# Kernel tuning notes

Measured on AMD Instinct MI355X. Metric: run time of the kernel, lower is better.

## Reference

```python
import jax, jax.numpy as jnp
import numpy as np

MAX_DEG = 6
N_ATOMS = 500000
BATCH = 1024
F_IN = 75
# atoms are sorted by degree (DeepChem ConvMol convention); counts for degree 0..6
DEG_COUNTS = [20000, 80000, 150000, 150000, 75000, 20000, 5000]
OFF = np.cumsum([0] + DEG_COUNTS)


def setup_inputs():
    key = jax.random.key(0)
    ks = jax.random.split(key, 20)

    def p(k, shape):
        return jax.random.normal(k, shape, jnp.float32) * 0.05

    inp = {}
    inp["atom_features"] = jax.random.normal(ks[0], (N_ATOMS, F_IN), jnp.float32)
    inp["membership"] = jax.random.randint(ks[1], (N_ATOMS,), 0, BATCH)
    for d in range(1, MAX_DEG + 1):
        inp[f"adj{d}"] = jax.random.randint(ks[1 + d], (DEG_COUNTS[d], d), 0, N_ATOMS)
    inp["gc1_Wn"] = p(ks[8], (MAX_DEG, F_IN, 64))
    inp["gc1_Ws"] = p(ks[9], (MAX_DEG + 1, F_IN, 64))
    inp["gc1_b"] = jnp.zeros((MAX_DEG + 1, 64), jnp.float32)
    inp["gc2_Wn"] = p(ks[10], (MAX_DEG, 64, 64))
    inp["gc2_Ws"] = p(ks[11], (MAX_DEG + 1, 64, 64))
    inp["gc2_b"] = jnp.zeros((MAX_DEG + 1, 64), jnp.float32)
    inp["bn1_gamma"] = jnp.ones((64,), jnp.float32)
    inp["bn1_beta"] = jnp.zeros((64,), jnp.float32)
    inp["bn1_mean"] = jnp.zeros((64,), jnp.float32)
    inp["bn1_var"] = jnp.ones((64,), jnp.float32)
    inp["bn3_gamma"] = jnp.ones((128,), jnp.float32)
    inp["bn3_beta"] = jnp.zeros((128,), jnp.float32)
    inp["bn3_mean"] = jnp.zeros((128,), jnp.float32)
    inp["bn3_var"] = jnp.ones((128,), jnp.float32)
    inp["d1_W"] = p(ks[12], (64, 128))
    inp["d1_b"] = jnp.zeros((128,), jnp.float32)
    inp["d2_W"] = p(ks[13], (256, 64))
    inp["d2_b"] = jnp.zeros((64,), jnp.float32)
    inp["d3_W"] = p(ks[14], (64, 1))
    inp["d3_b"] = jnp.zeros((1,), jnp.float32)
    return inp


def batch_norm(x, gamma, beta, mean, var, eps=1e-3):
    # keras BatchNormalization in inference mode (eps = keras default 1e-3)
    return gamma * (x - mean) * jax.lax.rsqrt(var + eps) + beta


def graph_conv(feat, adjs, Wn, Ws, b):
    # degree-0 atoms: self transform only
    outs = [feat[OFF[0]:OFF[1]] @ Ws[0] + b[0]]
    for d in range(1, MAX_DEG + 1):
        summed = feat[adjs[d - 1]].sum(axis=1)        # [n_d, F] neighbor-sum gather
        self_a = feat[OFF[d]:OFF[d + 1]]              # [n_d, F] atoms of degree d
        outs.append(summed @ Wn[d - 1] + self_a @ Ws[d] + b[d])
    return jnp.tanh(jnp.concatenate(outs, axis=0))


def graph_pool(feat, adjs):
    outs = [feat[OFF[0]:OFF[1]]]                      # degree-0: passthrough
    for d in range(1, MAX_DEG + 1):
        gathered = feat[adjs[d - 1]]                  # [n_d, d, F]
        self_a = feat[OFF[d]:OFF[d + 1]][:, None, :]  # [n_d, 1, F]
        outs.append(jnp.max(jnp.concatenate([self_a, gathered], axis=1), axis=1))
    return jnp.concatenate(outs, axis=0)


def graph_gather(feat, membership):
    s = jax.ops.segment_sum(feat, membership, num_segments=BATCH)
    m = jax.ops.segment_max(feat, membership, num_segments=BATCH)
    return jnp.tanh(jnp.concatenate([s, m], axis=1))  # [BATCH, 2F]


def reference(atom_features, membership, adj1, adj2, adj3, adj4, adj5, adj6,
              gc1_Wn, gc1_Ws, gc1_b, gc2_Wn, gc2_Ws, gc2_b,
              bn1_gamma, bn1_beta, bn1_mean, bn1_var,
              bn3_gamma, bn3_beta, bn3_mean, bn3_var,
              d1_W, d1_b, d2_W, d2_b, d3_W, d3_b):
    adjs = [adj1, adj2, adj3, adj4, adj5, adj6]
    h = graph_conv(atom_features, adjs, gc1_Wn, gc1_Ws, gc1_b)
    h = batch_norm(h, bn1_gamma, bn1_beta, bn1_mean, bn1_var)
    h = graph_pool(h, adjs)
    h = graph_conv(h, adjs, gc2_Wn, gc2_Ws, gc2_b)
    # NOTE: source code reuses self.batch_norm1 after gc2 (batch_norm2 is unused)
    h = batch_norm(h, bn1_gamma, bn1_beta, bn1_mean, bn1_var)
    h = graph_pool(h, adjs)
    h = jnp.tanh(h @ d1_W + d1_b)
    h = batch_norm(h, bn3_gamma, bn3_beta, bn3_mean, bn3_var)
    g = graph_gather(h, membership)                   # [BATCH, 256]
    g = jax.nn.sigmoid(g @ d2_W + d2_b)
    return g @ d3_W + d3_b                            # [BATCH, 1]
```

## Files before the change

### kernel.cpp

```cpp
#include <hip/hip_runtime.h>
#include <hip/hip_fp16.h>
#include <math.h>


struct AdjPtrs { const int* p[6]; };

typedef _Float16 f16x8 __attribute__((ext_vector_type(8)));
typedef float f32x4 __attribute__((ext_vector_type(4)));

__device__ __forceinline__ float tanh_fast(float x) {
  float ax = fabsf(x);
  float r = __expf(-2.f * ax);
  float t = 1.f - 2.f * r * __builtin_amdgcn_rcpf(1.f + r);
  return copysignf(t, x);
}

__device__ __forceinline__ f16x8 max8(f16x8 a, f16x8 b) {
  #pragma unroll
  for (int i = 0; i < 8; i++) a[i] = (a[i] > b[i]) ? a[i] : b[i];
  return a;
}

__global__ __launch_bounds__(256) void k_zero_hist(int* __restrict__ hist) {
  int i = blockIdx.x * 256 + threadIdx.x;
  if (i < 1024) hist[i] = 0;
}

__global__ __launch_bounds__(256) void k_hist(const int* __restrict__ mem, int* __restrict__ hist) {
  __shared__ int lh[1024];
  int tid = threadIdx.x;
  for (int i = tid; i < 1024; i += 256) lh[i] = 0;
  __syncthreads();
  int stride = gridDim.x * 256;
  for (int i = blockIdx.x * 256 + tid; i < 500000; i += stride)
    atomicAdd(&lh[mem[i]], 1);
  __syncthreads();
  for (int i = tid; i < 1024; i += 256) {
    int v = lh[i];
    if (v) atomicAdd(&hist[i], v);
  }
}

__global__ __launch_bounds__(1024) void k_scan(const int* __restrict__ hist,
                                               int* __restrict__ start,
                                               int* __restrict__ cursor) {
  __shared__ int sc[1024];
  int t = threadIdx.x;
  int h = hist[t];
  sc[t] = h;
  __syncthreads();
  for (int off = 1; off < 1024; off <<= 1) {
    int v = (t >= off) ? sc[t - off] : 0;
    __syncthreads();
    sc[t] += v;
    __syncthreads();
  }
  int ex = sc[t] - h;
  start[t] = ex;
  cursor[t] = ex;
}

__global__ __launch_bounds__(256) void k_scatter(const int* __restrict__ mem,
                                                 int* __restrict__ cursor,
                                                 int* __restrict__ list) {
  int i = blockIdx.x * 256 + threadIdx.x;
  if (i < 500000) {
    int pos = atomicAdd(&cursor[mem[i]], 1);
    list[pos] = i;
  }
}

__global__ __launch_bounds__(256) void k_prep(const float* __restrict__ feat,
                                              __half2* __restrict__ featH2) {
  int i = blockIdx.x * 256 + threadIdx.x;
  int a = i / 40;
  int jp = i - a * 40;
  int kk = jp * 2;
  float v0 = (kk < 75) ? feat[(size_t)a * 75 + kk] : 0.f;
  float v1 = (kk + 1 < 75) ? feat[(size_t)a * 75 + kk + 1] : 0.f;
  featH2[i] = __floats2half2_rn(v0, v1);
}

__global__ __launch_bounds__(256) void k_prep_w(
    const float* __restrict__ Ws1, const float* __restrict__ Wn1,
    const float* __restrict__ Ws2, const float* __restrict__ Wn2,
    __half* __restrict__ W1H, __half* __restrict__ W2H) {
  int i = blockIdx.x * 256 + threadIdx.x;
  if (i < 71680) {
    int d = i / 10240, r = i - d * 10240;
    int j = r & 7, lane = (r >> 3) & 63, t = r >> 9;
    int n = (t & 3) * 16 + (lane & 15);
    int k = (t >> 2) * 32 + (lane >> 4) * 8 + j;
    float v = 0.f;
    if (k < 75) v = Ws1[d * 4800 + k * 64 + n];
    else if (k >= 80 && k < 155 && d > 0) v = Wn1[(d - 1) * 4800 + (k - 80) * 64 + n];
    W1H[i] = __float2half(v);
  } else {
    int i2 = i - 71680;
    int d = i2 / 8192, r = i2 - d * 8192;
    int j = r & 7, lane = (r >> 3) & 63, t = r >> 9;
    int n = (t & 3) * 16 + (lane & 15);
    int k = (t >> 2) * 32 + (lane >> 4) * 8 + j;
    float v = 0.f;
    if (k < 64) v = Ws2[d * 4096 + k * 64 + n];
    else if (d > 0) v = Wn2[(d - 1) * 4096 + (k - 64) * 64 + n];
    W2H[i2] = __float2half(v);
  }
}

__global__ __launch_bounds__(256) void k_prep_d1(const float* __restrict__ W,
                                                 __half* __restrict__ D1H) {
  int i = blockIdx.x * 256 + threadIdx.x;
  int n = i >> 6, k = i & 63;
  float v = W[k * 128 + n];
  __half hi = __float2half(v);
  D1H[i] = hi;
  D1H[8192 + i] = __float2half(v - __half2float(hi));
}

template<int FP, int NCH, int D>
__device__ __forceinline__ void gcm_run(
    const __half* __restrict__ featH, const int* __restrict__ adj_g,
    int abase, int na, const f16x8* __restrict__ Wf,
    const float* __restrict__ bias_d,
    const float* __restrict__ bng, const float* __restrict__ bnb,
    const float* __restrict__ bnm, const float* __restrict__ bnv,
    __half* __restrict__ out) {
  int tid = threadIdx.x;
  int lane = tid & 63, w = tid >> 6;
  int ln = lane & 15, q = lane >> 4;

  int ar[2][D > 0 ? D : 1];
  if (D > 0) {
    #pragma unroll
    for (int ms = 0; ms < 2; ms++) {
      int m = w * 32 + ms * 16 + ln;
      bool ok = (m < na);
      #pragma unroll
      for (int e = 0; e < D; e++)
        ar[ms][e] = ok ? adj_g[m * D + e] : 0;
    }
  }

  f32x4 acc[2][4];
  #pragma unroll
  for (int ns = 0; ns < 4; ns++) {
    float bj = bias_d[ns * 16 + ln];
    acc[0][ns] = (f32x4){bj, bj, bj, bj};
    acc[1][ns] = acc[0][ns];
  }

  #pragma unroll
  for (int c = 0; c < NCH; c++) {
    int ksg = c * 32 + q * 8;
    f16x8 af[2];
    #pragma unroll
    for (int ms = 0; ms < 2; ms++) {
      int m = w * 32 + ms * 16 + ln;
      if (ksg < FP) {
        af[ms] = *(const f16x8*)(featH + (size_t)(abase + m) * FP + ksg);
      } else if (D > 0) {
        int kb = ksg - FP;
        f16x8 v = *(const f16x8*)(featH + (size_t)ar[ms][0] * FP + kb);
        #pragma unroll
        for (int e = 1; e < D; e++) {
          f16x8 u = *(const f16x8*)(featH + (size_t)ar[ms][e] * FP + kb);
          v = v + u;
        }
        af[ms] = v;
      } else {
        af[ms] = (f16x8){};
      }
    }
    #pragma unroll
    for (int ns = 0; ns < 4; ns++) {
      f16x8 bf = Wf[(c * 4 + ns) * 64 + lane];
      acc[0][ns] = __builtin_amdgcn_mfma_f32_16x16x32_f16(af[0], bf, acc[0][ns], 0, 0, 0);
      acc[1][ns] = __builtin_amdgcn_mfma_f32_16x16x32_f16(af[1], bf, acc[1][ns], 0, 0, 0);
    }
  }

  #pragma unroll
  for (int ns = 0; ns < 4; ns++) {
    int j = ns * 16 + ln;
    float scv = bng[j] * rsqrtf(bnv[j] + 1e-3f);
    float shv = bnb[j] - bnm[j] * scv;
    #pragma unroll
    for (int ms = 0; ms < 2; ms++) {
      #pragma unroll
      for (int r = 0; r < 4; r++) {
        int atom = w * 32 + ms * 16 + q * 4 + r;
        if (atom < na)
          out[(size_t)(abase + atom) * 64 + j] =
              __float2half(tanh_fast(acc[ms][ns][r]) * scv + shv);
      }
    }
  }
}

template<int FP, int NCH>
__global__ __launch_bounds__(256, 4) void k_gcm(
    const __half* __restrict__ featH, AdjPtrs adjs,
    const __half* __restrict__ WtH, const float* __restrict__ bias,
    const float* __restrict__ bng, const float* __restrict__ bnb,
    const float* __restrict__ bnm, const float* __restrict__ bnv,
    __half* __restrict__ out) {
  int bid = blockIdx.x;
  int d, off, end, bloc;
  if      (bid < 157)  { d = 0; bloc = bid;        off = 0;      end = 20000;  }
  else if (bid < 782)  { d = 1; bloc = bid - 157;  off = 20000;  end = 100000; }
  else if (bid < 1954) { d = 2; bloc = bid - 782;  off = 100000; end = 250000; }
  else if (bid < 3126) { d = 3; bloc = bid - 1954; off = 250000; end = 400000; }
  else if (bid < 3712) { d = 4; bloc = bid - 3126; off = 400000; end = 475000; }
  else if (bid < 3869) { d = 5; bloc = bid - 3712; off = 475000; end = 495000; }
  else                 { d = 6; bloc = bid - 3869; off = 495000; end = 500000; }
  int abase = off + bloc * 128;
  int na = min(128, end - abase);
  const int* adj_g = (d > 0) ? adjs.p[d - 1] + (abase - off) * d : (const int*)0;
  const f16x8* Wf = (const f16x8*)WtH + d * (NCH * 4 * 64);
  const float* bias_d = bias + d * 64;

  switch (d) {
    case 0: gcm_run<FP, NCH, 0>(featH, adj_g, abase, na, Wf, bias_d, bng, bnb, bnm, bnv, out); break;
    case 1: gcm_run<FP, NCH, 1>(featH, adj_g, abase, na, Wf, bias_d, bng, bnb, bnm, bnv, out); break;
    case 2: gcm_run<FP, NCH, 2>(featH, adj_g, abase, na, Wf, bias_d, bng, bnb, bnm, bnv, out); break;
    case 3: gcm_run<FP, NCH, 3>(featH, adj_g, abase, na, Wf, bias_d, bng, bnb, bnm, bnv, out); break;
    case 4: gcm_run<FP, NCH, 4>(featH, adj_g, abase, na, Wf, bias_d, bng, bnb, bnm, bnv, out); break;
    case 5: gcm_run<FP, NCH, 5>(featH, adj_g, abase, na, Wf, bias_d, bng, bnb, bnm, bnv, out); break;
    default: gcm_run<FP, NCH, 6>(featH, adj_g, abase, na, Wf, bias_d, bng, bnb, bnm, bnv, out); break;
  }
}

template<int D>
__device__ __forceinline__ f16x8 pool_h_acc(const f16x8* __restrict__ in8,
                                            const int* __restrict__ ad, int sg, f16x8 v) {
  #pragma unroll
  for (int e = 0; e < D; e++) v = max8(v, in8[ad[e] * 8 + sg]);
  return v;
}

__global__ __launch_bounds__(256) void k_pool_h(const f16x8* __restrict__ in8, AdjPtrs adjs,
                                                f16x8* __restrict__ out8) {
  int t = blockIdx.x * 256 + threadIdx.x;
  int atom = t >> 3, sg = t & 7;
  int d, off;
  if      (atom < 20000)  { d = 0; off = 0;      }
  else if (atom < 100000) { d = 1; off = 20000;  }
  else if (atom < 250000) { d = 2; off = 100000; }
  else if (atom < 400000) { d = 3; off = 250000; }
  else if (atom < 475000) { d = 4; off = 400000; }
  else if (atom < 495000) { d = 5; off = 475000; }
  else                    { d = 6; off = 495000; }
  f16x8 v = in8[atom * 8 + sg];
  if (d > 0) {
    const int* ad = adjs.p[d - 1] + (atom - off) * d;
    switch (d) {
      case 1: v = pool_h_acc<1>(in8, ad, sg, v); break;
      case 2: v = pool_h_acc<2>(in8, ad, sg, v); break;
      case 3: v = pool_h_acc<3>(in8, ad, sg, v); break;
      case 4: v = pool_h_acc<4>(in8, ad, sg, v); break;
      case 5: v = pool_h_acc<5>(in8, ad, sg, v); break;
      default: v = pool_h_acc<6>(in8, ad, sg, v); break;
    }
  }
  out8[atom * 8 + sg] = v;
}

__global__ __launch_bounds__(256, 3) void k_dense1f(
    const __half2* __restrict__ hD2, const int* __restrict__ list,
    const int* __restrict__ start, const int* __restrict__ hist,
    const __half* __restrict__ D1H, const float* __restrict__ d1b,
    const float* __restrict__ g3, const float* __restrict__ b3,
    const float* __restrict__ m3, const float* __restrict__ v3,
    float* __restrict__ g) {
  __shared__ __align__(16) __half Bt[2][128 * 72];
  __shared__ __align__(16) __half Ac[64 * 72];
  int b = blockIdx.x, tid = threadIdx.x;
  int stt = start[b], cnt = hist[b];

  for (int i = tid; i < 8192; i += 256) {
    int n = i >> 6, k = i & 63;
    Bt[0][n * 72 + k] = D1H[i];
    Bt[1][n * 72 + k] = D1H[8192 + i];
  }

  int lane = tid & 63, w = tid >> 6;
  int ln = lane & 15, q = lane >> 4;

  float bj[2], sc[2], sh[2];
  #pragma unroll
  for (int nf = 0; nf < 2; nf++) {
    int col = w * 32 + nf * 16 + ln;
    bj[nf] = d1b[col];
    sc[nf] = g3[col] * rsqrtf(v3[col] + 1e-3f);
    sh[nf] = b3[col] - m3[col] * sc[nf];
  }

  float sum[2] = {0.f, 0.f};
  float mx[2] = {-INFINITY, -INFINITY};

  for (int cb = 0; cb < cnt; cb += 64) {
    int nr = min(64, cnt - cb);
    __syncthreads();
    {
      int r = tid >> 2;
      #pragma unroll
      for (int it = 0; it < 2; it++) {
        int sg = (tid & 3) + it * 4;
        __half2* dst = (__half2*)(Ac + r * 72 + sg * 8);
        if (r < nr) {
          int a = list[stt + cb + r];
          const __half2* src = hD2 + (size_t)a * 32 + sg * 4;
          __half2 v0 = src[0], v1 = src[1], v2 = src[2], v3h = src[3];
          dst[0] = v0; dst[1] = v1; dst[2] = v2; dst[3] = v3h;
        } else {
          __half2 z = __floats2half2_rn(0.f, 0.f);
          dst[0] = z; dst[1] = z; dst[2] = z; dst[3] = z;
        }
      }
    }
    __syncthreads();

    f32x4 acc[4][2];
    #pragma unroll
    for (int mf = 0; mf < 4; mf++)
      #pragma unroll
      for (int nf = 0; nf < 2; nf++) acc[mf][nf] = (f32x4){bj[nf], bj[nf], bj[nf], bj[nf]};

    #pragma unroll
    for (int hl = 1; hl >= 0; hl--) {
      #pragma unroll
      for (int ks = 0; ks < 2; ks++) {
        f16x8 af[4], bf[2];
        #pragma unroll
        for (int mf = 0; mf < 4; mf++)
          af[mf] = *(const f16x8*)(Ac + (mf * 16 + ln) * 72 + ks * 32 + q * 8);
        #pragma unroll
        for (int nf = 0; nf < 2; nf++)
          bf[nf] = *(const f16x8*)(&Bt[hl][(w * 32 + nf * 16 + ln) * 72 + ks * 32 + q * 8]);
        #pragma unroll
        for (int mf = 0; mf < 4; mf++)
          #pragma unroll
          for (int nf = 0; nf < 2; nf++)
            acc[mf][nf] = __builtin_amdgcn_mfma_f32_16x16x32_f16(af[mf], bf[nf], acc[mf][nf], 0, 0, 0);
      }
    }

    #pragma unroll
    for (int mf = 0; mf < 4; mf++) {
      #pragma unroll
      for (int nf = 0; nf < 2; nf++) {
        #pragma unroll
        for (int r = 0; r < 4; r++) {
          int row = mf * 16 + q * 4 + r;
          if (row < nr) {
            float v = tanh_fast(acc[mf][nf][r]) * sc[nf] + sh[nf];
            sum[nf] += v;
            mx[nf] = fmaxf(mx[nf], v);
          }
        }
      }
    }
  }

  #pragma unroll
  for (int nf = 0; nf < 2; nf++) {
    sum[nf] += __shfl_xor(sum[nf], 16);
    sum[nf] += __shfl_xor(sum[nf], 32);
    mx[nf] = fmaxf(mx[nf], __shfl_xor(mx[nf], 16));
    mx[nf] = fmaxf(mx[nf], __shfl_xor(mx[nf], 32));
  }
  if (q == 0) {
    #pragma unroll
    for (int nf = 0; nf < 2; nf++) {
      int col = w * 32 + nf * 16 + ln;
      g[b * 256 + col] = tanh_fast(sum[nf]);
      g[b * 256 + 128 + col] = tanh_fast(mx[nf]);
    }
  }
}

__global__ __launch_bounds__(64) void k_dense23(
    const float* __restrict__ g, const float* __restrict__ W2,
    const float* __restrict__ b2, const float* __restrict__ W3,
    const float* __restrict__ b3, float* __restrict__ out) {
  __shared__ float gr[256];
  int b = blockIdx.x, j = threadIdx.x;
  ((float4*)gr)[j] = ((const float4*)(g + b * 256))[j];
  __syncthreads();
  float acc = b2[j];
  #pragma unroll 8
  for (int k = 0; k < 256; k++) acc += gr[k] * W2[k * 64 + j];
  float sg = 1.f / (1.f + expf(-acc));
  float p = sg * W3[j];
  #pragma unroll
  for (int off = 32; off >= 1; off >>= 1) p += __shfl_xor(p, off);
  if (j == 0) out[b] = p + b3[0];
}

extern "C" void kernel_launch(void* const* d_in, const int* in_sizes, int n_in,
                              void* d_out, int out_size, void* d_ws, size_t ws_size,
                              hipStream_t stream) {
  const float* feat = (const float*)d_in[0];
  const int*   mem  = (const int*)d_in[1];
  AdjPtrs adjs;
  for (int i = 0; i < 6; i++) adjs.p[i] = (const int*)d_in[2 + i];
  const float* gc1_Wn = (const float*)d_in[8];
  const float* gc1_Ws = (const float*)d_in[9];
  const float* gc1_b  = (const float*)d_in[10];
  const float* gc2_Wn = (const float*)d_in[11];
  const float* gc2_Ws = (const float*)d_in[12];
  const float* gc2_b  = (const float*)d_in[13];
  const float* bn1g = (const float*)d_in[14];
  const float* bn1b = (const float*)d_in[15];
  const float* bn1m = (const float*)d_in[16];
  const float* bn1v = (const float*)d_in[17];
  const float* bn3g = (const float*)d_in[18];
  const float* bn3b = (const float*)d_in[19];
  const float* bn3m = (const float*)d_in[20];
  const float* bn3v = (const float*)d_in[21];
  const float* d1W = (const float*)d_in[22];
  const float* d1b = (const float*)d_in[23];
  const float* d2W = (const float*)d_in[24];
  const float* d2b = (const float*)d_in[25];
  const float* d3W = (const float*)d_in[26];
  const float* d3b = (const float*)d_in[27];
  float* out = (float*)d_out;

  char* w = (char*)d_ws;
  __half* featH = (__half*)(w);
  __half* hA    = (__half*)(w + 80000000LL);
  __half* hB    = (__half*)(w + 144000000LL);
  __half* hC    = (__half*)(w);
  __half* hD    = (__half*)(w + 80000000LL);
  __half* W1H   = (__half*)(w + 210000000LL);
  __half* W2H   = (__half*)(w + 210200000LL);
  __half* D1H   = (__half*)(w + 210330000LL);
  float*  g     = (float*)(w + 210400000LL);
  int* hist     = (int*)(w + 211600000LL);
  int* start    = (int*)(w + 211604096LL);
  int* cursor   = (int*)(w + 211608192LL);
  int* list     = (int*)(w + 211612288LL);

  k_zero_hist<<<4, 256, 0, stream>>>(hist);
  k_hist<<<512, 256, 0, stream>>>(mem, hist);
  k_scan<<<1, 1024, 0, stream>>>(hist, start, cursor);
  k_scatter<<<1954, 256, 0, stream>>>(mem, cursor, list);

  k_prep<<<78125, 256, 0, stream>>>(feat, (__half2*)featH);
  k_prep_w<<<504, 256, 0, stream>>>(gc1_Ws, gc1_Wn, gc2_Ws, gc2_Wn, W1H, W2H);
  k_prep_d1<<<32, 256, 0, stream>>>(d1W, D1H);

  k_gcm<80, 5><<<3909, 256, 0, stream>>>(featH, adjs, W1H, gc1_b,
                                         bn1g, bn1b, bn1m, bn1v, hA);
  k_pool_h<<<15625, 256, 0, stream>>>((const f16x8*)hA, adjs, (f16x8*)hB);
  k_gcm<64, 4><<<3909, 256, 0, stream>>>(hB, adjs, W2H, gc2_b,
                                         bn1g, bn1b, bn1m, bn1v, hC);
  k_pool_h<<<15625, 256, 0, stream>>>((const f16x8*)hC, adjs, (f16x8*)hD);
  k_dense1f<<<1024, 256, 0, stream>>>((const __half2*)hD, list, start, hist, D1H, d1b,
                                      bn3g, bn3b, bn3m, bn3v, g);
  k_dense23<<<1024, 64, 0, stream>>>(g, d2W, d2b, d3W, d3b, out);
}
```

Baseline: 707.6 us.

## Halve gcm tile to 64 atoms and drop LDS staging in dense1f

The graph-conv kernel now processes 16 atoms per wave (64 per block) instead of 32. That halves register use for accumulators and adjacency indices, doubles the grid and raises the occupancy hint from 4 to 6 blocks per CU, so more gathers are in flight. The dense1 kernel no longer stages the weight matrix and gathered rows through shared memory. Each wave reads rows and weights straight from global memory with no barriers, relying on cache hits instead of LDS. This cuts LDS use and sync overhead, but the weights are reloaded from global per chunk and each weight fetch feeds fewer MFMAs.

After: 688.5 us. 2.7% less time.

```diff
diff --git a/kernel.cpp b/kernel.cpp
--- a/kernel.cpp
+++ b/kernel.cpp
@@ -129,54 +129,44 @@
   int tid = threadIdx.x;
   int lane = tid & 63, w = tid >> 6;
   int ln = lane & 15, q = lane >> 4;
-
-  int ar[2][D > 0 ? D : 1];
+  int m = w * 16 + ln;
+
+  int ar[D > 0 ? D : 1];
   if (D > 0) {
-    #pragma unroll
-    for (int ms = 0; ms < 2; ms++) {
-      int m = w * 32 + ms * 16 + ln;
-      bool ok = (m < na);
-      #pragma unroll
-      for (int e = 0; e < D; e++)
-        ar[ms][e] = ok ? adj_g[m * D + e] : 0;
-    }
-  }
-
-  f32x4 acc[2][4];
+    bool ok = (m < na);
+    #pragma unroll
+    for (int e = 0; e < D; e++) ar[e] = ok ? adj_g[m * D + e] : 0;
+  }
+
+  f32x4 acc[4];
   #pragma unroll
   for (int ns = 0; ns < 4; ns++) {
     float bj = bias_d[ns * 16 + ln];
-    acc[0][ns] = (f32x4){bj, bj, bj, bj};
-    acc[1][ns] = acc[0][ns];
+    acc[ns] = (f32x4){bj, bj, bj, bj};
   }
 
   #pragma unroll
   for (int c = 0; c < NCH; c++) {
     int ksg = c * 32 + q * 8;
-    f16x8 af[2];
-    #pragma unroll
-    for (int ms = 0; ms < 2; ms++) {
-      int m = w * 32 + ms * 16 + ln;
-      if (ksg < FP) {
-        af[ms] = *(const f16x8*)(featH + (size_t)(abase + m) * FP + ksg);
-      } else if (D > 0) {
-        int kb = ksg - FP;
-        f16x8 v = *(const f16x8*)(featH + (size_t)ar[ms][0] * FP + kb);
-        #pragma unroll
-        for (int e = 1; e < D; e++) {
-          f16x8 u = *(const f16x8*)(featH + (size_t)ar[ms][e] * FP + kb);
-          v = v + u;
-        }
-        af[ms] = v;
-      } else {
-        af[ms] = (f16x8){};
+    f16x8 af;
+    if (ksg < FP) {
+      af = *(const f16x8*)(featH + (size_t)(abase + m) * FP + ksg);
+    } else if (D > 0) {
+      int kb = ksg - FP;
+      f16x8 v = *(const f16x8*)(featH + (size_t)ar[0] * FP + kb);
+      #pragma unroll
+      for (int e = 1; e < D; e++) {
+        f16x8 u = *(const f16x8*)(featH + (size_t)ar[e] * FP + kb);
+        v = v + u;
       }
+      af = v;
+    } else {
+      af = (f16x8){};
     }
     #pragma unroll
     for (int ns = 0; ns < 4; ns++) {
       f16x8 bf = Wf[(c * 4 + ns) * 64 + lane];
-      acc[0][ns] = __builtin_amdgcn_mfma_f32_16x16x32_f16(af[0], bf, acc[0][ns], 0, 0, 0);
-      acc[1][ns] = __builtin_amdgcn_mfma_f32_16x16x32_f16(af[1], bf, acc[1][ns], 0, 0, 0);
+      acc[ns] = __builtin_amdgcn_mfma_f32_16x16x32_f16(af, bf, acc[ns], 0, 0, 0);
     }
   }
 
@@ -186,20 +176,17 @@
     float scv = bng[j] * rsqrtf(bnv[j] + 1e-3f);
     float shv = bnb[j] - bnm[j] * scv;
     #pragma unroll
-    for (int ms = 0; ms < 2; ms++) {
-      #pragma unroll
-      for (int r = 0; r < 4; r++) {
-        int atom = w * 32 + ms * 16 + q * 4 + r;
-        if (atom < na)
-          out[(size_t)(abase + atom) * 64 + j] =
-              __float2half(tanh_fast(acc[ms][ns][r]) * scv + shv);
-      }
+    for (int r = 0; r < 4; r++) {
+      int atom = w * 16 + q * 4 + r;
+      if (atom < na)
+        out[(size_t)(abase + atom) * 64 + j] =
+            __float2half(tanh_fast(acc[ns][r]) * scv + shv);
     }
   }
 }
 
 template<int FP, int NCH>
-__global__ __launch_bounds__(256, 4) void k_gcm(
+__global__ __launch_bounds__(256, 6) void k_gcm(
     const __half* __restrict__ featH, AdjPtrs adjs,
     const __half* __restrict__ WtH, const float* __restrict__ bias,
     const float* __restrict__ bng, const float* __restrict__ bnb,
@@ -207,15 +194,15 @@
     __half* __restrict__ out) {
   int bid = blockIdx.x;
   int d, off, end, bloc;
-  if      (bid < 157)  { d = 0; bloc = bid;        off = 0;      end = 20000;  }
-  else if (bid < 782)  { d = 1; bloc = bid - 157;  off = 20000;  end = 100000; }
-  else if (bid < 1954) { d = 2; bloc = bid - 782;  off = 100000; end = 250000; }
-  else if (bid < 3126) { d = 3; bloc = bid - 1954; off = 250000; end = 400000; }
-  else if (bid < 3712) { d = 4; bloc = bid - 3126; off = 400000; end = 475000; }
-  else if (bid < 3869) { d = 5; bloc = bid - 3712; off = 475000; end = 495000; }
-  else                 { d = 6; bloc = bid - 3869; off = 495000; end = 500000; }
-  int abase = off + bloc * 128;
-  int na = min(128, end - abase);
+  if      (bid < 313)  { d = 0; bloc = bid;        off = 0;      end = 20000;  }
+  else if (bid < 1563) { d = 1; bloc = bid - 313;  off = 20000;  end = 100000; }
+  else if (bid < 3907) { d = 2; bloc = bid - 1563; off = 100000; end = 250000; }
+  else if (bid < 6251) { d = 3; bloc = bid - 3907; off = 250000; end = 400000; }
+  else if (bid < 7423) { d = 4; bloc = bid - 6251; off = 400000; end = 475000; }
+  else if (bid < 7736) { d = 5; bloc = bid - 7423; off = 475000; end = 495000; }
+  else                 { d = 6; bloc = bid - 7736; off = 495000; end = 500000; }
+  int abase = off + bloc * 64;
+  int na = min(64, end - abase);
   const int* adj_g = (d > 0) ? adjs.p[d - 1] + (abase - off) * d : (const int*)0;
   const f16x8* Wf = (const f16x8*)WtH + d * (NCH * 4 * 64);
   const float* bias_d = bias + d * 64;
@@ -266,26 +253,17 @@
   out8[atom * 8 + sg] = v;
 }
 
-__global__ __launch_bounds__(256, 3) void k_dense1f(
-    const __half2* __restrict__ hD2, const int* __restrict__ list,
+__global__ __launch_bounds__(256, 4) void k_dense1f(
+    const __half* __restrict__ hD, const int* __restrict__ list,
     const int* __restrict__ start, const int* __restrict__ hist,
     const __half* __restrict__ D1H, const float* __restrict__ d1b,
     const float* __restrict__ g3, const float* __restrict__ b3,
     const float* __restrict__ m3, const float* __restrict__ v3,
     float* __restrict__ g) {
-  __shared__ __align__(16) __half Bt[2][128 * 72];
-  __shared__ __align__(16) __half Ac[64 * 72];
   int b = blockIdx.x, tid = threadIdx.x;
-  int stt = start[b], cnt = hist[b];
-
-  for (int i = tid; i < 8192; i += 256) {
-    int n = i >> 6, k = i & 63;
-    Bt[0][n * 72 + k] = D1H[i];
-    Bt[1][n * 72 + k] = D1H[8192 + i];
-  }
-
   int lane = tid & 63, w = tid >> 6;
   int ln = lane & 15, q = lane >> 4;
+  int stt = start[b], cnt = hist[b];
 
   float bj[2], sc[2], sh[2];
   #pragma unroll
@@ -301,25 +279,12 @@
 
   for (int cb = 0; cb < cnt; cb += 64) {
     int nr = min(64, cnt - cb);
-    __syncthreads();
-    {
-      int r = tid >> 2;
-      #pragma unroll
-      for (int it = 0; it < 2; it++) {
-        int sg = (tid & 3) + it * 4;
-        __half2* dst = (__half2*)(Ac + r * 72 + sg * 8);
-        if (r < nr) {
-          int a = list[stt + cb + r];
-          const __half2* src = hD2 + (size_t)a * 32 + sg * 4;
-          __half2 v0 = src[0], v1 = src[1], v2 = src[2], v3h = src[3];
-          dst[0] = v0; dst[1] = v1; dst[2] = v2; dst[3] = v3h;
-        } else {
-          __half2 z = __floats2half2_rn(0.f, 0.f);
-          dst[0] = z; dst[1] = z; dst[2] = z; dst[3] = z;
-        }
-      }
-    }
-    __syncthreads();
+    int ridx[4];
+    #pragma unroll
+    for (int mf = 0; mf < 4; mf++) {
+      int row = mf * 16 + ln;
+      ridx[mf] = list[stt + cb + min(row, nr - 1)];
+    }
 
     f32x4 acc[4][2];
     #pragma unroll
@@ -331,18 +296,18 @@
     for (int hl = 1; hl >= 0; hl--) {
       #pragma unroll
       for (int ks = 0; ks < 2; ks++) {
-        f16x8 af[4], bf[2];
+        f16x8 af[4];
         #pragma unroll
         for (int mf = 0; mf < 4; mf++)
-          af[mf] = *(const f16x8*)(Ac + (mf * 16 + ln) * 72 + ks * 32 + q * 8);
+          af[mf] = *(const f16x8*)(hD + (size_t)ridx[mf] * 64 + ks * 32 + q * 8);
         #pragma unroll
-        for (int nf = 0; nf < 2; nf++)
-          bf[nf] = *(const f16x8*)(&Bt[hl][(w * 32 + nf * 16 + ln) * 72 + ks * 32 + q * 8]);
-        #pragma unroll
-        for (int mf = 0; mf < 4; mf++)
+        for (int nf = 0; nf < 2; nf++) {
+          f16x8 bf = *(const f16x8*)(D1H + hl * 8192 +
+                                     (w * 32 + nf * 16 + ln) * 64 + ks * 32 + q * 8);
           #pragma unroll
-          for (int nf = 0; nf < 2; nf++)
-            acc[mf][nf] = __builtin_amdgcn_mfma_f32_16x16x32_f16(af[mf], bf[nf], acc[mf][nf], 0, 0, 0);
+          for (int mf = 0; mf < 4; mf++)
+            acc[mf][nf] = __builtin_amdgcn_mfma_f32_16x16x32_f16(af[mf], bf, acc[mf][nf], 0, 0, 0);
+        }
       }
     }
 
@@ -451,13 +416,13 @@
   k_prep_w<<<504, 256, 0, stream>>>(gc1_Ws, gc1_Wn, gc2_Ws, gc2_Wn, W1H, W2H);
   k_prep_d1<<<32, 256, 0, stream>>>(d1W, D1H);
 
-  k_gcm<80, 5><<<3909, 256, 0, stream>>>(featH, adjs, W1H, gc1_b,
+  k_gcm<80, 5><<<7815, 256, 0, stream>>>(featH, adjs, W1H, gc1_b,
                                          bn1g, bn1b, bn1m, bn1v, hA);
   k_pool_h<<<15625, 256, 0, stream>>>((const f16x8*)hA, adjs, (f16x8*)hB);
-  k_gcm<64, 4><<<3909, 256, 0, stream>>>(hB, adjs, W2H, gc2_b,
+  k_gcm<64, 4><<<7815, 256, 0, stream>>>(hB, adjs, W2H, gc2_b,
                                          bn1g, bn1b, bn1m, bn1v, hC);
   k_pool_h<<<15625, 256, 0, stream>>>((const f16x8*)hC, adjs, (f16x8*)hD);
-  k_dense1f<<<1024, 256, 0, stream>>>((const __half2*)hD, list, start, hist, D1H, d1b,
+  k_dense1f<<<1024, 256, 0, stream>>>((const __half*)hD, list, start, hist, D1H, d1b,
                                       bn3g, bn3b, bn3m, bn3v, g);
   k_dense23<<<1024, 64, 0, stream>>>(g, d2W, d2b, d3W, d3b, out);
 }
```
